# Performance work log

Measured on AMD Instinct MI355X. Metric: run time of the kernel, lower is better.

## Reference

```python
import jax, jax.numpy as jnp
import numpy as np

NEG_SLOPE = 0.2  # PyG GATConv default leaky_relu negative_slope
BN_EPS = 1e-5


def gat_layer(x, src, dst, W, a_src, a_dst, bias):
    """PyG-style GATConv (self-loops already appended to src/dst).
    x: [N, F_in], W: [F_in, H*C], a_src/a_dst: [H, C], bias: [H*C].
    Returns [N, H*C] (concat heads)."""
    N = x.shape[0]
    H, C = a_src.shape
    h = (x @ W).reshape(N, H, C)                      # [N, H, C]
    al_src = jnp.sum(h * a_src[None], axis=-1)        # [N, H]
    al_dst = jnp.sum(h * a_dst[None], axis=-1)        # [N, H]
    e = jax.nn.leaky_relu(al_src[src] + al_dst[dst], NEG_SLOPE)  # [E, H]
    # segment softmax over destination neighborhoods
    m = jax.ops.segment_max(e, dst, num_segments=N)   # [N, H]
    ee = jnp.exp(e - m[dst])
    denom = jax.ops.segment_sum(ee, dst, num_segments=N)  # [N, H]
    alpha = ee / denom[dst]                           # [E, H]
    out = jax.ops.segment_sum(alpha[:, :, None] * h[src], dst, num_segments=N)  # [N, H, C]
    return out.reshape(N, H * C) + bias


def batch_norm(x, gamma, beta):
    mu = jnp.mean(x, axis=0)
    var = jnp.var(x, axis=0)  # biased, matches torch BN training stats
    return gamma * (x - mu) * jax.lax.rsqrt(var + BN_EPS) + beta


def setup_inputs() -> dict:
    key = jax.random.key(0)
    N, F, H, C = 50000, 128, 4, 64
    E = 400000
    HC = H * C  # 256
    ks = jax.random.split(key, 24)

    def glorot(k, shape, fan_in):
        return jax.random.normal(k, shape, dtype=jnp.float32) * (1.0 / np.sqrt(fan_in))

    inp = {
        "x": jax.random.normal(ks[0], (N, F), dtype=jnp.float32),
        "edge_index": jax.random.randint(ks[1], (2, E), 0, N, dtype=jnp.int64),
        # conv1: F -> H*C
        "W1": glorot(ks[2], (F, HC), F),
        "a1s": glorot(ks[3], (H, C), C),
        "a1d": glorot(ks[4], (H, C), C),
        "b1": jnp.zeros((HC,), jnp.float32),
        # conv2: H*C -> H*C
        "W2": glorot(ks[5], (HC, HC), HC),
        "a2s": glorot(ks[6], (H, C), C),
        "a2d": glorot(ks[7], (H, C), C),
        "b2": jnp.zeros((HC,), jnp.float32),
        # conv3: H*C -> C (1 head)
        "W3": glorot(ks[8], (HC, C), HC),
        "a3s": glorot(ks[9], (1, C), C),
        "a3d": glorot(ks[10], (1, C), C),
        "b3": jnp.zeros((C,), jnp.float32),
        # batch norms
        "g1": jnp.ones((HC,), jnp.float32),
        "be1": jnp.zeros((HC,), jnp.float32),
        "g2": jnp.ones((HC,), jnp.float32),
        "be2": jnp.zeros((HC,), jnp.float32),
        # MLP head: C -> C//2 -> 2
        "fw1": glorot(ks[11], (C, C // 2), C),
        "fb1": jnp.zeros((C // 2,), jnp.float32),
        "fw2": glorot(ks[12], (C // 2, 2), C // 2),
        "fb2": jnp.zeros((2,), jnp.float32),
    }
    return inp


def reference(x, edge_index, W1, a1s, a1d, b1, W2, a2s, a2d, b2,
              W3, a3s, a3d, b3, g1, be1, g2, be2, fw1, fb1, fw2, fb2):
    N = x.shape[0]
    loop = jnp.arange(N, dtype=edge_index.dtype)
    src = jnp.concatenate([edge_index[0], loop])  # self-loops (PyG default)
    dst = jnp.concatenate([edge_index[1], loop])

    h = gat_layer(x, src, dst, W1, a1s, a1d, b1)
    h = jax.nn.elu(batch_norm(h, g1, be1))
    h = gat_layer(h, src, dst, W2, a2s, a2d, b2)
    h = jax.nn.elu(batch_norm(h, g2, be2))
    h = jax.nn.elu(gat_layer(h, src, dst, W3, a3s, a3d, b3))
    h = jax.nn.relu(h @ fw1 + fb1)
    return h @ fw2 + fb2  # [N, 2] logits
```

## Files before the change

### kernel.cpp

```cpp
#include <hip/hip_runtime.h>
#include <math.h>
#include <stdint.h>

typedef __attribute__((ext_vector_type(8))) short short8v;
typedef __attribute__((ext_vector_type(4))) float float4v;

__device__ __forceinline__ float bf2f(unsigned short u) {
  return __uint_as_float((unsigned int)u << 16);
}
__device__ __forceinline__ unsigned short f2bf(float f) {
  unsigned int u = __float_as_uint(f);
  unsigned int r = (u + 0x7FFFu + ((u >> 16) & 1u)) >> 16;
  return (unsigned short)r;
}
__device__ __forceinline__ float exp_lrelu(float x) {
  x = x > 0.f ? x : 0.2f * x;
  return expf(x);
}

typedef __attribute__((address_space(3))) void lds_void;
typedef const __attribute__((address_space(1))) void glb_void;
__device__ __forceinline__ void gload_lds16(const void* g, void* l) {
  __builtin_amdgcn_global_load_lds((glb_void*)g, (lds_void*)l, 16, 0, 0);
}

__device__ __forceinline__ void wprep_one(const float* W, unsigned short* Wh,
                                          int t, int K, int Nw)
{
  int i = t & 7;
  int lane = (t >> 3) & 63;
  int frag = t >> 9;
  int ktiles = K >> 5;
  int n_tile = frag / ktiles, k_tile = frag - n_tile * ktiles;
  int k = k_tile * 32 + ((lane >> 4) << 3) + i;
  int n = (n_tile << 4) + (lane & 15);
  Wh[t] = f2bf(W[(size_t)k * Nw + n]);
}

__global__ void wprep_all_kernel(const float* __restrict__ W1, unsigned short* __restrict__ w1h,
                                 const float* __restrict__ W2, unsigned short* __restrict__ w2h,
                                 const float* __restrict__ W3, unsigned short* __restrict__ w3h)
{
  int t = blockIdx.x * 256 + threadIdx.x;
  const int s1 = 128 * 256, s2 = 256 * 256, s3 = 256 * 64;
  if (t < s1) { wprep_one(W1, w1h, t, 128, 256); return; }
  t -= s1;
  if (t < s2) { wprep_one(W2, w2h, t, 256, 256); return; }
  t -= s2;
  if (t < s3) { wprep_one(W3, w3h, t, 256, 64); }
}

__global__ __launch_bounds__(256) void split_kernel(const float* __restrict__ in,
    unsigned short* __restrict__ hi, size_t n4)
{
  size_t i0 = (size_t)blockIdx.x * 256 + threadIdx.x;
  size_t stride = (size_t)gridDim.x * 256;
  for (size_t idx = i0; idx < n4; idx += stride) {
    float4 v = ((const float4*)in)[idx];
    ushort4 h;
    h.x = f2bf(v.x); h.y = f2bf(v.y); h.z = f2bf(v.z); h.w = f2bf(v.w);
    ((ushort4*)hi)[idx] = h;
  }
}

__global__ __launch_bounds__(256) void bnsplit_kernel(const unsigned short* __restrict__ act,
    const float* __restrict__ scale, const float* __restrict__ shift,
    unsigned short* __restrict__ hi, size_t nchunks)
{
  size_t i0 = (size_t)blockIdx.x * 256 + threadIdx.x;
  size_t stride = (size_t)gridDim.x * 256;
  for (size_t idx = i0; idx < nchunks; idx += stride) {
    ushort4 u = ((const ushort4*)act)[idx];
    int f = (int)((idx * 4) & 255);
    float4 sc = *(const float4*)(scale + f);
    float4 sh = *(const float4*)(shift + f);
    float v0 = fmaf(bf2f(u.x), sc.x, sh.x);
    float v1 = fmaf(bf2f(u.y), sc.y, sh.y);
    float v2 = fmaf(bf2f(u.z), sc.z, sh.z);
    float v3 = fmaf(bf2f(u.w), sc.w, sh.w);
    v0 = v0 > 0.f ? v0 : expm1f(v0);
    v1 = v1 > 0.f ? v1 : expm1f(v1);
    v2 = v2 > 0.f ? v2 : expm1f(v2);
    v3 = v3 > 0.f ? v3 : expm1f(v3);
    ushort4 h;
    h.x = f2bf(v0); h.y = f2bf(v1); h.z = f2bf(v2); h.w = f2bf(v3);
    ((ushort4*)hi)[idx] = h;
  }
}

template<int MI, int WM, int WN, int KSTEPS, int HEADS>
__global__ __launch_bounds__(128) void gemm_al(
    const unsigned short* __restrict__ Ah, const unsigned short* __restrict__ Bh,
    const float* __restrict__ a_s, const float* __restrict__ a_d,
    unsigned short* __restrict__ C, float* __restrict__ al_s, float* __restrict__ al_d,
    int M)
{
  constexpr int NWAVES = WM * WN;
  constexpr int BM = WM * MI * 16;
  constexpr int TILEB = BM * 64 * 2;
  constexpr int Nw = HEADS * 64;
  constexpr int K = KSTEPS * 64;
  constexpr int KT32 = KSTEPS * 2;
  __shared__ __align__(16) unsigned char smem[2][TILEB];

  const int wid = threadIdx.x >> 6, lane = threadIdx.x & 63;
  const int wm = wid / WN, wn = wid % WN;
  const int gn = blockIdx.y * WN + wn;
  const int m0 = blockIdx.x * BM;
  const int n0 = gn * 64;
  const int ar = lane & 15;
  const int cchunk = lane >> 4;
  const int ntile0 = n0 >> 4;

  float4v acc[MI][4];
#pragma unroll
  for (int mi = 0; mi < MI; ++mi)
#pragma unroll
    for (int ni = 0; ni < 4; ++ni)
      acc[mi][ni] = (float4v){0.f, 0.f, 0.f, 0.f};

  auto stage = [&](int buf, int ks) {
#pragma unroll
    for (int c = wid; c < 8; c += NWAVES) {
      const unsigned short* gp = Ah + (size_t)(m0 + lane) * K + ks * 64 + c * 8;
      gload_lds16(gp, &smem[buf][c * 1024 + lane * 16]);
    }
  };

  stage(0, 0);
  int cur = 0;
  for (int ks = 0; ks < KSTEPS; ++ks) {
    __syncthreads();
    short8v bh[2][4];
#pragma unroll
    for (int hh = 0; hh < 2; ++hh)
#pragma unroll
      for (int ni = 0; ni < 4; ++ni) {
        int kt = ks * 2 + hh;
        size_t off = (((size_t)(ntile0 + ni) * KT32 + kt) * 64 + lane) * 8;
        bh[hh][ni] = *(const short8v*)(Bh + off);
      }
    if (ks + 1 < KSTEPS) stage(cur ^ 1, ks + 1);
    short8v ah[2][MI];
#pragma unroll
    for (int hh = 0; hh < 2; ++hh)
#pragma unroll
      for (int mi = 0; mi < MI; ++mi) {
        int row = wm * MI * 16 + mi * 16 + ar;
        int c = hh * 4 + cchunk;
        ah[hh][mi] = *(const short8v*)&smem[cur][c * 1024 + row * 16];
      }
#pragma unroll
    for (int hh = 0; hh < 2; ++hh)
#pragma unroll
      for (int mi = 0; mi < MI; ++mi)
#pragma unroll
        for (int ni = 0; ni < 4; ++ni)
          acc[mi][ni] = __builtin_amdgcn_mfma_f32_16x16x32_bf16(ah[hh][mi], bh[hh][ni], acc[mi][ni], 0, 0, 0);
    cur ^= 1;
  }

  const int cc = lane & 15;
#pragma unroll
  for (int mi = 0; mi < MI; ++mi) {
    int rowb = m0 + wm * MI * 16 + mi * 16 + ((lane >> 4) << 2);
#pragma unroll
    for (int r = 0; r < 4; ++r) {
      int row = rowb + r;
      if (row < M) {
#pragma unroll
        for (int ni = 0; ni < 4; ++ni)
          C[(size_t)row * Nw + n0 + ni * 16 + cc] = f2bf(acc[mi][ni][r]);
      }
    }
  }

  const int head = (HEADS == 4) ? gn : 0;
  float as_[4], ad_[4];
#pragma unroll
  for (int ni = 0; ni < 4; ++ni) {
    as_[ni] = a_s[head * 64 + ni * 16 + cc];
    ad_[ni] = a_d[head * 64 + ni * 16 + cc];
  }
#pragma unroll
  for (int mi = 0; mi < MI; ++mi) {
#pragma unroll
    for (int r = 0; r < 4; ++r) {
      float h0 = bf2f(f2bf(acc[mi][0][r]));
      float h1 = bf2f(f2bf(acc[mi][1][r]));
      float h2 = bf2f(f2bf(acc[mi][2][r]));
      float h3 = bf2f(f2bf(acc[mi][3][r]));
      float ps = h0 * as_[0] + h1 * as_[1] + h2 * as_[2] + h3 * as_[3];
      float pd = h0 * ad_[0] + h1 * ad_[1] + h2 * ad_[2] + h3 * ad_[3];
#pragma unroll
      for (int off = 1; off < 16; off <<= 1) {
        ps += __shfl_xor(ps, off);
        pd += __shfl_xor(pd, off);
      }
      int row = m0 + wm * MI * 16 + mi * 16 + ((lane >> 4) << 2) + r;
      if (cc == 0 && row < M) {
        al_s[row * HEADS + head] = ps;
        al_d[row * HEADS + head] = pd;
      }
    }
  }
}

__global__ void count_kernel(const int* __restrict__ dst, int E, int Etot, int* __restrict__ counts)
{
  int e = blockIdx.x * 256 + threadIdx.x;
  if (e >= Etot) return;
  int d = (e < E) ? dst[e] : (e - E);
  atomicAdd(&counts[d], 1);
}

__global__ void block_sum_kernel(const int* __restrict__ counts, int N, int* __restrict__ bsums)
{
  __shared__ int sd[256];
  int i = blockIdx.x * 256 + threadIdx.x;
  sd[threadIdx.x] = (i < N) ? counts[i] : 0;
  __syncthreads();
  for (int off = 128; off; off >>= 1) {
    if (threadIdx.x < off) sd[threadIdx.x] += sd[threadIdx.x + off];
    __syncthreads();
  }
  if (threadIdx.x == 0) bsums[blockIdx.x] = sd[0];
}

__global__ void scan_bsums_kernel(int* bsums, int nb)
{
  __shared__ int sd[256];
  int t = threadIdx.x;
  int v = (t < nb) ? bsums[t] : 0;
  sd[t] = v;
  __syncthreads();
  for (int off = 1; off < 256; off <<= 1) {
    int x = (t >= off) ? sd[t - off] : 0;
    __syncthreads();
    sd[t] += x;
    __syncthreads();
  }
  if (t < nb) bsums[t] = sd[t] - v;
}

__global__ void scan_write_kernel(const int* __restrict__ counts, int N,
                                  const int* __restrict__ bsums, int* __restrict__ rowStart, int Etot)
{
  __shared__ int sd[256];
  int i = blockIdx.x * 256 + threadIdx.x;
  int v = (i < N) ? counts[i] : 0;
  sd[threadIdx.x] = v;
  __syncthreads();
  for (int off = 1; off < 256; off <<= 1) {
    int x = (threadIdx.x >= off) ? sd[threadIdx.x - off] : 0;
    __syncthreads();
    sd[threadIdx.x] += x;
    __syncthreads();
  }
  if (i < N) rowStart[i] = bsums[blockIdx.x] + sd[threadIdx.x] - v;
  if (i == N - 1) rowStart[N] = Etot;
}

__global__ void fill_kernel(const int* __restrict__ src, const int* __restrict__ dst,
                            int E, int Etot, const int* __restrict__ rowStart,
                            int* __restrict__ cursor, int* __restrict__ csrSrc)
{
  int e = blockIdx.x * 256 + threadIdx.x;
  if (e >= Etot) return;
  int s, d;
  if (e < E) { s = src[e]; d = dst[e]; } else { s = d = e - E; }
  int pos = rowStart[d] + atomicAdd(&cursor[d], 1);
  csrSrc[pos] = s;
}

__global__ __launch_bounds__(256) void aggregate_fused4(
    const unsigned short* __restrict__ h16,
    const float* __restrict__ als, const float* __restrict__ ald,
    const int* __restrict__ csrSrc, const int* __restrict__ rowStart,
    unsigned short* __restrict__ outp, int N)
{
  __shared__ float ldsW[4][256];
  const int wl = threadIdx.x >> 6;
  int wid = blockIdx.x * 4 + wl;
  if (wid >= N) return;
  const int lane = threadIdx.x & 63;
  const int head = lane >> 4;
  const int start = rowStart[wid], end = rowStart[wid + 1];

  float4 adv = ((const float4*)ald)[wid];
  float acc[4] = {};
  float wsum = 0.f;

  for (int base = start; base < end; base += 64) {
    int cnt = end - base; if (cnt > 64) cnt = 64;
    int s_l = 0;
    if (lane < cnt) {
      s_l = csrSrc[base + lane];
      float4 av = ((const float4*)als)[s_l];
      float4 w4;
      w4.x = exp_lrelu(av.x + adv.x);
      w4.y = exp_lrelu(av.y + adv.y);
      w4.z = exp_lrelu(av.z + adv.z);
      w4.w = exp_lrelu(av.w + adv.w);
      *(float4*)&ldsW[wl][lane * 4] = w4;
    }
    int i = 0;
    for (; i + 4 <= cnt; i += 4) {
      int s0 = __shfl(s_l, i);
      int s1 = __shfl(s_l, i + 1);
      int s2 = __shfl(s_l, i + 2);
      int s3 = __shfl(s_l, i + 3);
      float w0 = ldsW[wl][(i + 0) * 4 + head];
      float w1 = ldsW[wl][(i + 1) * 4 + head];
      float w2 = ldsW[wl][(i + 2) * 4 + head];
      float w3 = ldsW[wl][(i + 3) * 4 + head];
      ushort4 r0 = ((const ushort4*)(h16 + (size_t)s0 * 256))[lane];
      ushort4 r1 = ((const ushort4*)(h16 + (size_t)s1 * 256))[lane];
      ushort4 r2 = ((const ushort4*)(h16 + (size_t)s2 * 256))[lane];
      ushort4 r3 = ((const ushort4*)(h16 + (size_t)s3 * 256))[lane];
      wsum += (w0 + w1) + (w2 + w3);
      acc[0] = fmaf(w0, bf2f(r0.x), acc[0]);
      acc[1] = fmaf(w0, bf2f(r0.y), acc[1]);
      acc[2] = fmaf(w0, bf2f(r0.z), acc[2]);
      acc[3] = fmaf(w0, bf2f(r0.w), acc[3]);
      acc[0] = fmaf(w1, bf2f(r1.x), acc[0]);
      acc[1] = fmaf(w1, bf2f(r1.y), acc[1]);
      acc[2] = fmaf(w1, bf2f(r1.z), acc[2]);
      acc[3] = fmaf(w1, bf2f(r1.w), acc[3]);
      acc[0] = fmaf(w2, bf2f(r2.x), acc[0]);
      acc[1] = fmaf(w2, bf2f(r2.y), acc[1]);
      acc[2] = fmaf(w2, bf2f(r2.z), acc[2]);
      acc[3] = fmaf(w2, bf2f(r2.w), acc[3]);
      acc[0] = fmaf(w3, bf2f(r3.x), acc[0]);
      acc[1] = fmaf(w3, bf2f(r3.y), acc[1]);
      acc[2] = fmaf(w3, bf2f(r3.z), acc[2]);
      acc[3] = fmaf(w3, bf2f(r3.w), acc[3]);
    }
    for (; i < cnt; ++i) {
      int s0 = __shfl(s_l, i);
      float w0 = ldsW[wl][i * 4 + head];
      wsum += w0;
      ushort4 r0 = ((const ushort4*)(h16 + (size_t)s0 * 256))[lane];
      acc[0] = fmaf(w0, bf2f(r0.x), acc[0]);
      acc[1] = fmaf(w0, bf2f(r0.y), acc[1]);
      acc[2] = fmaf(w0, bf2f(r0.z), acc[2]);
      acc[3] = fmaf(w0, bf2f(r0.w), acc[3]);
    }
  }

  float inv = 1.0f / wsum;
  ushort4 o;
  o.x = f2bf(acc[0] * inv); o.y = f2bf(acc[1] * inv);
  o.z = f2bf(acc[2] * inv); o.w = f2bf(acc[3] * inv);
  ((ushort4*)(outp + (size_t)wid * 256))[lane] = o;
}

__global__ __launch_bounds__(256) void agg3_mlp_kernel(
    const unsigned short* __restrict__ h16,
    const float* __restrict__ als, const float* __restrict__ ald,
    const int* __restrict__ csrSrc, const int* __restrict__ rowStart,
    const float* __restrict__ b3,
    const float* __restrict__ fw1, const float* __restrict__ fb1,
    const float* __restrict__ fw2, const float* __restrict__ fb2,
    float* __restrict__ out, int N)
{
  __shared__ float ldsW[4][64];
  __shared__ float w1s[64][32];
  __shared__ float mrow[4][64];
  const int t = threadIdx.x;
  for (int i = t; i < 2048; i += 256) w1s[i >> 5][i & 31] = fw1[i];
  __syncthreads();

  const int wl = t >> 6, lane = t & 63;
  const int j = lane & 31, col = lane >> 5;
  float w1c[64];
#pragma unroll
  for (int k = 0; k < 64; ++k) w1c[k] = w1s[k][j];
  const float b1v = fb1[j];
  const float w2v = fw2[j * 2 + col];
  const float b2v = fb2[col];
  const float b3v = b3[lane];

  const int nwaves = (int)gridDim.x * 4;
  for (int wid = blockIdx.x * 4 + wl; wid < N; wid += nwaves) {
    const int start = rowStart[wid], end = rowStart[wid + 1];
    const float ad0 = ald[wid];

    float acc = 0.f, wsum = 0.f;
    for (int base = start; base < end; base += 64) {
      int cnt = end - base; if (cnt > 64) cnt = 64;
      int s_l = 0;
      if (lane < cnt) {
        s_l = csrSrc[base + lane];
        ldsW[wl][lane] = exp_lrelu(als[s_l] + ad0);
      }
      int i = 0;
      for (; i + 4 <= cnt; i += 4) {
        int s0 = __shfl(s_l, i);
        int s1 = __shfl(s_l, i + 1);
        int s2 = __shfl(s_l, i + 2);
        int s3 = __shfl(s_l, i + 3);
        float w0 = ldsW[wl][i + 0];
        float w1 = ldsW[wl][i + 1];
        float w2 = ldsW[wl][i + 2];
        float w3 = ldsW[wl][i + 3];
        unsigned short r0 = h16[(size_t)s0 * 64 + lane];
        unsigned short r1 = h16[(size_t)s1 * 64 + lane];
        unsigned short r2 = h16[(size_t)s2 * 64 + lane];
        unsigned short r3 = h16[(size_t)s3 * 64 + lane];
        wsum += (w0 + w1) + (w2 + w3);
        acc = fmaf(w0, bf2f(r0), acc);
        acc = fmaf(w1, bf2f(r1), acc);
        acc = fmaf(w2, bf2f(r2), acc);
        acc = fmaf(w3, bf2f(r3), acc);
      }
      for (; i < cnt; ++i) {
        int s0 = __shfl(s_l, i);
        float w0 = ldsW[wl][i];
        wsum += w0;
        unsigned short r0 = h16[(size_t)s0 * 64 + lane];
        acc = fmaf(w0, bf2f(r0), acc);
      }
    }
    float o = acc / wsum + b3v;
    o = o > 0.f ? o : expm1f(o);

    mrow[wl][lane] = o;
    float hid = b1v;
#pragma unroll
    for (int k = 0; k < 64; ++k)
      hid = fmaf(mrow[wl][k], w1c[k], hid);
    hid = fmaxf(hid, 0.f);
    float p = hid * w2v;
#pragma unroll
    for (int off = 1; off < 32; off <<= 1) p += __shfl_xor(p, off);
    if (j == 0) out[(size_t)wid * 2 + col] = p + b2v;
  }
}

__global__ __launch_bounds__(256) void bn_stats_kernel(const unsigned short* __restrict__ x, int N,
                                float* __restrict__ partials)
{
  const int wid = threadIdx.x >> 6, lane = threadIdx.x & 63;
  const int gw = blockIdx.x * 4 + wid;
  const int tw = gridDim.x * 4;
  float4 s = make_float4(0.f, 0.f, 0.f, 0.f);
  float4 q = make_float4(0.f, 0.f, 0.f, 0.f);
#pragma unroll 4
  for (int r = gw; r < N; r += tw) {
    ushort4 u = ((const ushort4*)(x + (size_t)r * 256))[lane];
    float v0 = bf2f(u.x), v1 = bf2f(u.y), v2 = bf2f(u.z), v3 = bf2f(u.w);
    s.x += v0; s.y += v1; s.z += v2; s.w += v3;
    q.x = fmaf(v0, v0, q.x); q.y = fmaf(v1, v1, q.y);
    q.z = fmaf(v2, v2, q.z); q.w = fmaf(v3, v3, q.w);
  }
  __shared__ float ls[4][512];
  *(float4*)&ls[wid][lane * 4] = s;
  *(float4*)&ls[wid][256 + lane * 4] = q;
  __syncthreads();
  const int t = threadIdx.x;
  float a = ls[0][t] + ls[1][t] + ls[2][t] + ls[3][t];
  float b = ls[0][t + 256] + ls[1][t + 256] + ls[2][t + 256] + ls[3][t + 256];
  partials[blockIdx.x * 512 + t] = a;
  partials[blockIdx.x * 512 + 256 + t] = b;
}

__global__ void bn_final_kernel(const float* __restrict__ partials, int nblk,
                                const float* __restrict__ g, const float* __restrict__ be,
                                int N, float* __restrict__ scale, float* __restrict__ shift)
{
  int f = threadIdx.x;
  float s = 0.f, q = 0.f;
#pragma unroll 8
  for (int b = 0; b < nblk; ++b) {
    s += partials[b * 512 + f];
    q += partials[b * 512 + 256 + f];
  }
  float mu = s / N;
  float var = q / N - mu * mu;
  float rs = rsqrtf(var + 1e-5f);
  float sc = g[f] * rs;
  scale[f] = sc;
  shift[f] = be[f] - mu * sc;
}

extern "C" void kernel_launch(void* const* d_in, const int* in_sizes, int n_in,
                              void* d_out, int out_size, void* d_ws, size_t ws_size,
                              hipStream_t stream)
{
  const float* x   = (const float*)d_in[0];
  const int*   ei  = (const int*)d_in[1];
  const float* W1  = (const float*)d_in[2];
  const float* a1s = (const float*)d_in[3];
  const float* a1d = (const float*)d_in[4];
  const float* W2  = (const float*)d_in[6];
  const float* a2s = (const float*)d_in[7];
  const float* a2d = (const float*)d_in[8];
  const float* W3  = (const float*)d_in[10];
  const float* a3s = (const float*)d_in[11];
  const float* a3d = (const float*)d_in[12];
  const float* b3  = (const float*)d_in[13];
  const float* g1  = (const float*)d_in[14];
  const float* be1 = (const float*)d_in[15];
  const float* g2  = (const float*)d_in[16];
  const float* be2 = (const float*)d_in[17];
  const float* fw1 = (const float*)d_in[18];
  const float* fb1 = (const float*)d_in[19];
  const float* fw2 = (const float*)d_in[20];
  const float* fb2 = (const float*)d_in[21];
  float* out = (float*)d_out;

  const int F = 128;
  const int N = in_sizes[0] / F;
  const int E = in_sizes[1] / 2;
  const int Etot = E + N;
  const int* srcIdx = ei;
  const int* dstIdx = ei + E;

  char* w = (char*)d_ws;
  auto alloc = [&](size_t bytes) -> void* {
    void* p = (void*)w;
    w += (bytes + 255) & ~(size_t)255;
    return p;
  };
  unsigned short* h16  = (unsigned short*)alloc((size_t)N * 256 * 2);
  unsigned short* act16= (unsigned short*)alloc((size_t)N * 256 * 2);
  unsigned short* aBf  = (unsigned short*)alloc((size_t)N * 256 * 2);
  float* als     = (float*)alloc((size_t)N * 4 * 4);
  float* ald     = (float*)alloc((size_t)N * 4 * 4);
  const size_t cntPad = ((size_t)N * 4 + 255) & ~(size_t)255;
  int*   counts  = (int*)alloc((size_t)N * 4);
  int*   cursor  = (int*)alloc((size_t)N * 4);
  int*   rowStart= (int*)alloc((size_t)(N + 1) * 4);
  int*   csrSrc  = (int*)alloc((size_t)Etot * 4);
  int*   bsums   = (int*)alloc((size_t)((N + 255) / 256) * 4);
  float* partials= (float*)alloc((size_t)128 * 512 * 4);
  float* scale1  = (float*)alloc(256 * 4);
  float* shift1  = (float*)alloc(256 * 4);
  float* scale2  = (float*)alloc(256 * 4);
  float* shift2  = (float*)alloc(256 * 4);
  unsigned short* w1h = (unsigned short*)alloc((size_t)128 * 256 * 2);
  unsigned short* w2h = (unsigned short*)alloc((size_t)256 * 256 * 2);
  unsigned short* w3h = (unsigned short*)alloc((size_t)256 * 64 * 2);
  (void)alloc(65536);

  const int nb = (N + 255) / 256;
  const int ebk = (Etot + 255) / 256;
  const int aggBlocks = (N + 3) / 4;

  const int wtot = 128 * 256 + 256 * 256 + 256 * 64;
  wprep_all_kernel<<<(wtot + 255) / 256, 256, 0, stream>>>(W1, w1h, W2, w2h, W3, w3h);

  hipMemsetAsync(counts, 0, cntPad + (size_t)N * 4, stream);
  count_kernel<<<ebk, 256, 0, stream>>>(dstIdx, E, Etot, counts);
  block_sum_kernel<<<nb, 256, 0, stream>>>(counts, N, bsums);
  scan_bsums_kernel<<<1, 256, 0, stream>>>(bsums, nb);
  scan_write_kernel<<<nb, 256, 0, stream>>>(counts, N, bsums, rowStart, Etot);
  fill_kernel<<<ebk, 256, 0, stream>>>(srcIdx, dstIdx, E, Etot, rowStart, cursor, csrSrc);

  dim3 g12((N + 63) / 64, 2);
  dim3 g3((N + 63) / 64, 1);

  split_kernel<<<2048, 256, 0, stream>>>(x, aBf, (size_t)N * 128 / 4);
  gemm_al<4, 1, 2, 2, 4><<<g12, 128, 0, stream>>>(aBf, w1h, a1s, a1d, h16, als, ald, N);
  aggregate_fused4<<<aggBlocks, 256, 0, stream>>>(h16, als, ald, csrSrc, rowStart, act16, N);
  bn_stats_kernel<<<128, 256, 0, stream>>>(act16, N, partials);
  bn_final_kernel<<<1, 256, 0, stream>>>(partials, 128, g1, be1, N, scale1, shift1);

  bnsplit_kernel<<<2048, 256, 0, stream>>>(act16, scale1, shift1, aBf, (size_t)N * 64);
  gemm_al<4, 1, 2, 4, 4><<<g12, 128, 0, stream>>>(aBf, w2h, a2s, a2d, h16, als, ald, N);
  aggregate_fused4<<<aggBlocks, 256, 0, stream>>>(h16, als, ald, csrSrc, rowStart, act16, N);
  bn_stats_kernel<<<128, 256, 0, stream>>>(act16, N, partials);
  bn_final_kernel<<<1, 256, 0, stream>>>(partials, 128, g2, be2, N, scale2, shift2);

  bnsplit_kernel<<<2048, 256, 0, stream>>>(act16, scale2, shift2, aBf, (size_t)N * 64);
  gemm_al<2, 2, 1, 4, 1><<<g3, 128, 0, stream>>>(aBf, w3h, a3s, a3d, h16, als, ald, N);
  agg3_mlp_kernel<<<2560, 256, 0, stream>>>(h16, als, ald, csrSrc, rowStart,
                                            b3, fw1, fb1, fw2, fb2, out, N);
}
```

Measured before the change: 312.1 us.

## Split neighbor gathers across half-waves with wider loads in aggregation kernels

In the 256-wide aggregation, each wave now processes two edges at once: each half-wave loads a 16-byte chunk per lane and the partial sums are combined with a cross-half shuffle. The 64-wide final aggregation processes four edges per iteration using 8-byte loads per lane. It also drops its grid-stride loop and 64-register weight cache for one node per wave, reading MLP weights from LDS. The aim is more memory-level parallelism and wider transactions per gather. The cost is extra shuffle reductions, idle lanes on short neighbor lists, and a larger launch for the final kernel.

```diff
diff --git a/kernel.cpp b/kernel.cpp
--- a/kernel.cpp
+++ b/kernel.cpp
@@ -284,11 +284,12 @@
   int wid = blockIdx.x * 4 + wl;
   if (wid >= N) return;
   const int lane = threadIdx.x & 63;
-  const int head = lane >> 4;
+  const int sub = lane >> 5, c = lane & 31;
+  const int head = c >> 3;
   const int start = rowStart[wid], end = rowStart[wid + 1];
 
   float4 adv = ((const float4*)ald)[wid];
-  float acc[4] = {};
+  float acc[8] = {};
   float wsum = 0.f;
 
   for (int base = start; base < end; base += 64) {
@@ -304,55 +305,28 @@
       w4.w = exp_lrelu(av.w + adv.w);
       *(float4*)&ldsW[wl][lane * 4] = w4;
     }
-    int i = 0;
-    for (; i + 4 <= cnt; i += 4) {
-      int s0 = __shfl(s_l, i);
-      int s1 = __shfl(s_l, i + 1);
-      int s2 = __shfl(s_l, i + 2);
-      int s3 = __shfl(s_l, i + 3);
-      float w0 = ldsW[wl][(i + 0) * 4 + head];
-      float w1 = ldsW[wl][(i + 1) * 4 + head];
-      float w2 = ldsW[wl][(i + 2) * 4 + head];
-      float w3 = ldsW[wl][(i + 3) * 4 + head];
-      ushort4 r0 = ((const ushort4*)(h16 + (size_t)s0 * 256))[lane];
-      ushort4 r1 = ((const ushort4*)(h16 + (size_t)s1 * 256))[lane];
-      ushort4 r2 = ((const ushort4*)(h16 + (size_t)s2 * 256))[lane];
-      ushort4 r3 = ((const ushort4*)(h16 + (size_t)s3 * 256))[lane];
-      wsum += (w0 + w1) + (w2 + w3);
-      acc[0] = fmaf(w0, bf2f(r0.x), acc[0]);
-      acc[1] = fmaf(w0, bf2f(r0.y), acc[1]);
-      acc[2] = fmaf(w0, bf2f(r0.z), acc[2]);
-      acc[3] = fmaf(w0, bf2f(r0.w), acc[3]);
-      acc[0] = fmaf(w1, bf2f(r1.x), acc[0]);
-      acc[1] = fmaf(w1, bf2f(r1.y), acc[1]);
-      acc[2] = fmaf(w1, bf2f(r1.z), acc[2]);
-      acc[3] = fmaf(w1, bf2f(r1.w), acc[3]);
-      acc[0] = fmaf(w2, bf2f(r2.x), acc[0]);
-      acc[1] = fmaf(w2, bf2f(r2.y), acc[1]);
-      acc[2] = fmaf(w2, bf2f(r2.z), acc[2]);
-      acc[3] = fmaf(w2, bf2f(r2.w), acc[3]);
-      acc[0] = fmaf(w3, bf2f(r3.x), acc[0]);
-      acc[1] = fmaf(w3, bf2f(r3.y), acc[1]);
-      acc[2] = fmaf(w3, bf2f(r3.z), acc[2]);
-      acc[3] = fmaf(w3, bf2f(r3.w), acc[3]);
-    }
-    for (; i < cnt; ++i) {
-      int s0 = __shfl(s_l, i);
-      float w0 = ldsW[wl][i * 4 + head];
-      wsum += w0;
-      ushort4 r0 = ((const ushort4*)(h16 + (size_t)s0 * 256))[lane];
-      acc[0] = fmaf(w0, bf2f(r0.x), acc[0]);
-      acc[1] = fmaf(w0, bf2f(r0.y), acc[1]);
-      acc[2] = fmaf(w0, bf2f(r0.z), acc[2]);
-      acc[3] = fmaf(w0, bf2f(r0.w), acc[3]);
-    }
-  }
-
-  float inv = 1.0f / wsum;
-  ushort4 o;
-  o.x = f2bf(acc[0] * inv); o.y = f2bf(acc[1] * inv);
-  o.z = f2bf(acc[2] * inv); o.w = f2bf(acc[3] * inv);
-  ((ushort4*)(outp + (size_t)wid * 256))[lane] = o;
+    for (int i = 0; i < cnt; i += 2) {
+      int e = i + sub;
+      int s = __shfl(s_l, e);
+      float w = (e < cnt) ? ldsW[wl][e * 4 + head] : 0.f;
+      short8v r = *(const short8v*)(h16 + (size_t)s * 256 + c * 8);
+      wsum += w;
+#pragma unroll
+      for (int q = 0; q < 8; ++q)
+        acc[q] = fmaf(w, bf2f((unsigned short)r[q]), acc[q]);
+    }
+  }
+#pragma unroll
+  for (int q = 0; q < 8; ++q) acc[q] += __shfl_xor(acc[q], 32);
+  wsum += __shfl_xor(wsum, 32);
+
+  if (sub == 0) {
+    float inv = 1.0f / wsum;
+    short8v o;
+#pragma unroll
+    for (int q = 0; q < 8; ++q) o[q] = (short)f2bf(acc[q] * inv);
+    *(short8v*)(outp + (size_t)wid * 256 + c * 8) = o;
+  }
 }
 
 __global__ __launch_bounds__(256) void agg3_mlp_kernel(
@@ -372,70 +346,65 @@
   __syncthreads();
 
   const int wl = t >> 6, lane = t & 63;
+  const int sub = lane >> 4, c = lane & 15;
   const int j = lane & 31, col = lane >> 5;
-  float w1c[64];
-#pragma unroll
-  for (int k = 0; k < 64; ++k) w1c[k] = w1s[k][j];
   const float b1v = fb1[j];
   const float w2v = fw2[j * 2 + col];
   const float b2v = fb2[col];
-  const float b3v = b3[lane];
-
-  const int nwaves = (int)gridDim.x * 4;
-  for (int wid = blockIdx.x * 4 + wl; wid < N; wid += nwaves) {
-    const int start = rowStart[wid], end = rowStart[wid + 1];
-    const float ad0 = ald[wid];
-
-    float acc = 0.f, wsum = 0.f;
-    for (int base = start; base < end; base += 64) {
-      int cnt = end - base; if (cnt > 64) cnt = 64;
-      int s_l = 0;
-      if (lane < cnt) {
-        s_l = csrSrc[base + lane];
-        ldsW[wl][lane] = exp_lrelu(als[s_l] + ad0);
-      }
-      int i = 0;
-      for (; i + 4 <= cnt; i += 4) {
-        int s0 = __shfl(s_l, i);
-        int s1 = __shfl(s_l, i + 1);
-        int s2 = __shfl(s_l, i + 2);
-        int s3 = __shfl(s_l, i + 3);
-        float w0 = ldsW[wl][i + 0];
-        float w1 = ldsW[wl][i + 1];
-        float w2 = ldsW[wl][i + 2];
-        float w3 = ldsW[wl][i + 3];
-        unsigned short r0 = h16[(size_t)s0 * 64 + lane];
-        unsigned short r1 = h16[(size_t)s1 * 64 + lane];
-        unsigned short r2 = h16[(size_t)s2 * 64 + lane];
-        unsigned short r3 = h16[(size_t)s3 * 64 + lane];
-        wsum += (w0 + w1) + (w2 + w3);
-        acc = fmaf(w0, bf2f(r0), acc);
-        acc = fmaf(w1, bf2f(r1), acc);
-        acc = fmaf(w2, bf2f(r2), acc);
-        acc = fmaf(w3, bf2f(r3), acc);
-      }
-      for (; i < cnt; ++i) {
-        int s0 = __shfl(s_l, i);
-        float w0 = ldsW[wl][i];
-        wsum += w0;
-        unsigned short r0 = h16[(size_t)s0 * 64 + lane];
-        acc = fmaf(w0, bf2f(r0), acc);
-      }
-    }
-    float o = acc / wsum + b3v;
-    o = o > 0.f ? o : expm1f(o);
-
-    mrow[wl][lane] = o;
-    float hid = b1v;
-#pragma unroll
-    for (int k = 0; k < 64; ++k)
-      hid = fmaf(mrow[wl][k], w1c[k], hid);
-    hid = fmaxf(hid, 0.f);
-    float p = hid * w2v;
-#pragma unroll
-    for (int off = 1; off < 32; off <<= 1) p += __shfl_xor(p, off);
-    if (j == 0) out[(size_t)wid * 2 + col] = p + b2v;
-  }
+  const float4 b3q = ((const float4*)b3)[c];
+
+  int wid = blockIdx.x * 4 + wl;
+  if (wid >= N) return;
+  const int start = rowStart[wid], end = rowStart[wid + 1];
+  const float ad0 = ald[wid];
+
+  float a0 = 0.f, a1 = 0.f, a2 = 0.f, a3 = 0.f, wsum = 0.f;
+  for (int base = start; base < end; base += 64) {
+    int cnt = end - base; if (cnt > 64) cnt = 64;
+    int s_l = 0;
+    if (lane < cnt) {
+      s_l = csrSrc[base + lane];
+      ldsW[wl][lane] = exp_lrelu(als[s_l] + ad0);
+    }
+    for (int i = 0; i < cnt; i += 4) {
+      int e = i + sub;
+      int s = __shfl(s_l, e);
+      float w = (e < cnt) ? ldsW[wl][e] : 0.f;
+      ushort4 r = ((const ushort4*)(h16 + (size_t)s * 64))[c];
+      wsum += w;
+      a0 = fmaf(w, bf2f(r.x), a0);
+      a1 = fmaf(w, bf2f(r.y), a1);
+      a2 = fmaf(w, bf2f(r.z), a2);
+      a3 = fmaf(w, bf2f(r.w), a3);
+    }
+  }
+  a0 += __shfl_xor(a0, 16); a1 += __shfl_xor(a1, 16);
+  a2 += __shfl_xor(a2, 16); a3 += __shfl_xor(a3, 16);
+  wsum += __shfl_xor(wsum, 16);
+  a0 += __shfl_xor(a0, 32); a1 += __shfl_xor(a1, 32);
+  a2 += __shfl_xor(a2, 32); a3 += __shfl_xor(a3, 32);
+  wsum += __shfl_xor(wsum, 32);
+
+  float inv = 1.0f / wsum;
+  float o0 = fmaf(a0, inv, 0.f) + b3q.x;
+  float o1 = fmaf(a1, inv, 0.f) + b3q.y;
+  float o2 = fmaf(a2, inv, 0.f) + b3q.z;
+  float o3 = fmaf(a3, inv, 0.f) + b3q.w;
+  o0 = o0 > 0.f ? o0 : expm1f(o0);
+  o1 = o1 > 0.f ? o1 : expm1f(o1);
+  o2 = o2 > 0.f ? o2 : expm1f(o2);
+  o3 = o3 > 0.f ? o3 : expm1f(o3);
+  if (sub == 0) *(float4*)&mrow[wl][c * 4] = make_float4(o0, o1, o2, o3);
+
+  float hid = b1v;
+#pragma unroll
+  for (int k = 0; k < 64; ++k)
+    hid = fmaf(mrow[wl][k], w1s[k][j], hid);
+  hid = fmaxf(hid, 0.f);
+  float p = hid * w2v;
+#pragma unroll
+  for (int off = 1; off < 32; off <<= 1) p += __shfl_xor(p, off);
+  if (j == 0) out[(size_t)wid * 2 + col] = p + b2v;
 }
 
 __global__ __launch_bounds__(256) void bn_stats_kernel(const unsigned short* __restrict__ x, int N,
@@ -575,6 +544,6 @@
 
   bnsplit_kernel<<<2048, 256, 0, stream>>>(act16, scale2, shift2, aBf, (size_t)N * 64);
   gemm_al<2, 2, 1, 4, 1><<<g3, 128, 0, stream>>>(aBf, w3h, a3s, a3d, h16, als, ald, N);
-  agg3_mlp_kernel<<<2560, 256, 0, stream>>>(h16, als, ald, csrSrc, rowStart,
-                                            b3, fw1, fb1, fw2, fb2, out, N);
-}
+  agg3_mlp_kernel<<<aggBlocks, 256, 0, stream>>>(h16, als, ald, csrSrc, rowStart,
+                                                 b3, fw1, fb1, fw2, fb2, out, N);
+}
```

After: 309.8 us. No clear change (-0.7%).
